# Kernel tuning notes

Hardware: AMD Instinct MI355X
Metric: run time of the kernel (lower is better)

Reference implementation:

```python
import jax, jax.numpy as jnp
import numpy as np
from jax import lax

B = 1024          # batch size (queries / docs)
H = 1536          # GRU hidden = embedding dim (hard-coded in module)
MAX_NEGS = 32     # max negatives per query
TEMP = 0.05       # opt.temperature


def setup_inputs() -> dict:
    key = jax.random.key(0)
    ks = jax.random.split(key, 8)
    rng = np.random.default_rng(0)
    lens = rng.integers(0, MAX_NEGS + 1, size=B)  # variable-length negs, some zero
    total = int(lens.sum())
    s = 0.02
    return {
        "q_emb": jax.random.normal(ks[0], (B, H), jnp.float32),
        "k_emb": jax.random.normal(ks[1], (B, H), jnp.float32),
        "inpn_emb": jax.random.normal(ks[2], (total, H), jnp.float32),
        "len_input_negs": jnp.asarray(lens, jnp.int32),
        "W_ih": jax.random.normal(ks[3], (3 * H, H), jnp.float32) * s,
        "W_hh": jax.random.normal(ks[4], (3 * H, H), jnp.float32) * s,
        "b_ih": jax.random.normal(ks[5], (3 * H,), jnp.float32) * s,
        "b_hh": jax.random.normal(ks[6], (3 * H,), jnp.float32) * s,
    }


def _ragged_gru_final(inpn_emb, lens, h0, W_ih, W_hh, b_ih, b_hh):
    """Batched equivalent of the per-sample torch GRU loop.

    For sample i: run a 1-layer GRU over inpn_emb[start_i:start_i+len_i]
    with initial hidden h0[i]; return final hidden (h0[i] if len_i == 0).
    """
    total = inpn_emb.shape[0]
    offsets = jnp.concatenate([jnp.zeros((1,), jnp.int32),
                               jnp.cumsum(lens)[:-1].astype(jnp.int32)])
    t = jnp.arange(MAX_NEGS, dtype=jnp.int32)
    idx = jnp.clip(offsets[:, None] + t[None, :], 0, total - 1)   # [B, Lmax]
    mask = t[None, :] < lens[:, None]                              # [B, Lmax]
    x_pad = inpn_emb[idx]                                          # [B, Lmax, H]

    def step(h, xm):
        x, m = xm                                  # x: [B,H], m: [B]
        gi = x @ W_ih.T + b_ih                     # [B, 3H]
        gh = h @ W_hh.T + b_hh                     # [B, 3H]
        i_r, i_z, i_n = jnp.split(gi, 3, axis=-1)
        h_r, h_z, h_n = jnp.split(gh, 3, axis=-1)
        r = jax.nn.sigmoid(i_r + h_r)
        z = jax.nn.sigmoid(i_z + h_z)
        n = jnp.tanh(i_n + r * h_n)
        h_new = (1.0 - z) * n + z * h
        h = jnp.where(m[:, None], h_new, h)        # freeze past end of seq
        return h, None

    h_final, _ = lax.scan(step, h0,
                          (x_pad.transpose(1, 0, 2), mask.T))
    return h_final


def reference(q_emb, k_emb, inpn_emb, len_input_negs, W_ih, W_hh, b_ih, b_hh):
    qemb = _ragged_gru_final(inpn_emb, len_input_negs, q_emb,
                             W_ih, W_hh, b_ih, b_hh)          # [B, H]
    scores = jnp.einsum("id,jd->ij", qemb / TEMP, k_emb)       # [B, B]
    labels = jnp.arange(B)
    logp = jax.nn.log_softmax(scores, axis=-1)
    loss = -jnp.mean(jnp.take_along_axis(logp, labels[:, None], axis=1))
    return loss
```

## Files before the change

### kernel.cpp

```cpp
#include <hip/hip_runtime.h>
#include <hip/hip_bf16.h>

#define B_SZ 1024
#define H_DIM 1536
#define H3 (3*H_DIM)
#define LMAX 32
#define TEMP_INV 20.0f

typedef __attribute__((ext_vector_type(4))) float f32x4;
typedef __attribute__((ext_vector_type(8))) short short8;
typedef unsigned short u16;
typedef unsigned int u32;

__device__ __forceinline__ u16 f2bf(float f){
  union { float f; u32 u; } v; v.f = f;
  u32 r = (v.u + 0x7FFFu + ((v.u >> 16) & 1u)) >> 16;
  return (u16)r;
}
__device__ __forceinline__ u32 pack2(float lo, float hi){
  return (u32)f2bf(lo) | ((u32)f2bf(hi) << 16);
}
__device__ __forceinline__ float bf2f(u16 b){
  union { u32 u; float f; } v; v.u = ((u32)b) << 16; return v.f;
}
__device__ __forceinline__ float sigm(float x){ return 1.f / (1.f + __expf(-x)); }

__device__ __forceinline__ void gload_lds16(const void* g, void* l){
  __builtin_amdgcn_global_load_lds(
      (const __attribute__((address_space(1))) void*)g,
      (__attribute__((address_space(3))) void*)l, 16, 0, 0);
}

__global__ void sort_kernel(const int* __restrict__ lens, int* __restrict__ rank,
                            int* __restrict__ cnt_arr, int* __restrict__ tstart,
                            int* __restrict__ rowmap)
{
  __shared__ int wavecnt[33][17];
  __shared__ int bintot[33];
  __shared__ int scnt[LMAX];
  __shared__ int sts[LMAX];
  __shared__ int soff[B_SZ];
  int i = threadIdx.x;
  int li = lens[i];
  int w = i >> 6, lane = i & 63;

  if (i < 33 * 17) ((int*)wavecnt)[i] = 0;
  __syncthreads();

  int mypre = 0;
  #pragma unroll 1
  for (int b = 0; b <= 32; ++b) {
    unsigned long long m = __ballot(li == b);
    if (lane == 0) wavecnt[b][w] = __popcll(m);
    if (b == li) mypre = __popcll(m & ((1ull << lane) - 1ull));
  }
  __syncthreads();

  if (i < 33) {
    int c = 0;
    #pragma unroll 1
    for (int w2 = 0; w2 < 16; ++w2) c += wavecnt[i][w2];
    bintot[i] = c;
  }
  __syncthreads();

  int wpre = 0;
  #pragma unroll 1
  for (int w2 = 0; w2 < w; ++w2) wpre += wavecnt[li][w2];
  int base = 0;
  #pragma unroll 1
  for (int b = li + 1; b <= 32; ++b) base += bintot[b];
  int r = base + wpre + mypre;
  rank[i] = r;

  if (i < LMAX) {
    int c = 0;
    #pragma unroll 1
    for (int b = i + 1; b <= 32; ++b) c += bintot[b];
    scnt[i] = c; cnt_arr[i] = c;
  }
  __syncthreads();
  if (i == 0) {
    int acc = 0;
    for (int t = 0; t < LMAX; ++t) { sts[t] = acc; tstart[t] = acc; acc += scnt[t]; }
  }

  soff[i] = li;
  __syncthreads();
  for (int off = 1; off < B_SZ; off <<= 1) {
    int v = (i >= off) ? soff[i - off] : 0;
    __syncthreads();
    soff[i] += v;
    __syncthreads();
  }
  int myoff = soff[i] - li;
  for (int t = 0; t < li; ++t)
    rowmap[myoff + t] = sts[t] + r;
}

__global__ void prep_kernel(const float* __restrict__ wih, const float* __restrict__ whh,
                            const float* __restrict__ kemb, const float* __restrict__ qemb,
                            const int* __restrict__ rank,
                            u16* __restrict__ wih_bf, u16* __restrict__ whh_bf,
                            u16* __restrict__ k_bf, u16* __restrict__ h0)
{
  size_t o = ((size_t)blockIdx.x * 256 + threadIdx.x) * 8;
  if (o < (size_t)H3 * H_DIM) {
    float4 a0 = *(const float4*)(wih + o), a1 = *(const float4*)(wih + o + 4);
    *(uint4*)(wih_bf + o) = make_uint4(pack2(a0.x,a0.y), pack2(a0.z,a0.w),
                                       pack2(a1.x,a1.y), pack2(a1.z,a1.w));
    float4 b0 = *(const float4*)(whh + o), b1 = *(const float4*)(whh + o + 4);
    *(uint4*)(whh_bf + o) = make_uint4(pack2(b0.x,b0.y), pack2(b0.z,b0.w),
                                       pack2(b1.x,b1.y), pack2(b1.z,b1.w));
  }
  if (o < (size_t)B_SZ * H_DIM) {
    float4 k0 = *(const float4*)(kemb + o), k1 = *(const float4*)(kemb + o + 4);
    *(uint4*)(k_bf + o) = make_uint4(pack2(k0.x,k0.y), pack2(k0.z,k0.w),
                                     pack2(k1.x,k1.y), pack2(k1.z,k1.w));
    int i = (int)(o / H_DIM), col = (int)(o % H_DIM);
    float4 q0 = *(const float4*)(qemb + o), q1 = *(const float4*)(qemb + o + 4);
    *(uint4*)(h0 + (size_t)rank[i] * H_DIM + col) =
        make_uint4(pack2(q0.x,q0.y), pack2(q0.z,q0.w),
                   pack2(q1.x,q1.y), pack2(q1.z,q1.w));
  }
}

__global__ void convx_kernel(const float* __restrict__ x, const int* __restrict__ rowmap,
                             u16* __restrict__ xt, int total){
  size_t o = ((size_t)blockIdx.x * 256 + threadIdx.x) * 8;
  int row = (int)(o / H_DIM), col = (int)(o % H_DIM);
  if (row < total) {
    float4 a0 = *(const float4*)(x + o), a1 = *(const float4*)(x + o + 4);
    *(uint4*)(xt + (size_t)rowmap[row] * H_DIM + col) =
        make_uint4(pack2(a0.x,a0.y), pack2(a0.z,a0.w),
                   pack2(a1.x,a1.y), pack2(a1.z,a1.w));
  } else {
    *(uint4*)(xt + o) = make_uint4(0,0,0,0);
  }
}

__global__ __launch_bounds__(256, 2) void gi_gemm_kernel(
    const u16* __restrict__ x_bf, const u16* __restrict__ wih_bf,
    const float* __restrict__ b_ih, u16* __restrict__ gi, int nblk_m)
{
  int nblk = nblk_m * 36;
  int id = blockIdx.x;
  int q8 = nblk >> 3, r8 = nblk & 7;
  int xcd = id & 7, off = id >> 3;
  int swz = (xcd < r8) ? (xcd * (q8 + 1) + off) : (r8 * (q8 + 1) + (xcd - r8) * q8 + off);
  int bx = swz / 36, by = swz % 36;

  __shared__ u16 lds[2 * 128 * 64];
  char* ldsb = (char*)lds;
  int tid = threadIdx.x, wid = tid >> 6, lane = tid & 63;
  int wm = wid >> 1, wn = wid & 1;
  int lrow = lane & 15, lkh = lane >> 4;
  f32x4 acc[4][4] = {};

  for (int kt = 0; kt < 24; ++kt) {
    int k0 = kt * 64;
    #pragma unroll
    for (int it = 0; it < 8; ++it) {
      int cb = it * 256 + wid * 64;
      int c  = cb + lane;
      int isB = c >> 10;
      int cc  = c & 1023;
      int row = cc >> 3, slot = cc & 7;
      const u16* src = isB ? (wih_bf + (size_t)(by * 128 + row) * H_DIM)
                           : (x_bf  + (size_t)(bx * 128 + row) * H_DIM);
      src += k0 + ((slot ^ (row & 7)) << 3);
      gload_lds16(src, ldsb + (size_t)cb * 16);
    }
    __syncthreads();
    #pragma unroll
    for (int qq = 0; qq < 2; ++qq) {
      short8 a[4], b[4];
      int slot = qq * 4 + lkh;
      #pragma unroll
      for (int m = 0; m < 4; ++m) {
        int row = wm * 64 + m * 16 + lrow;
        a[m] = *(const short8*)(ldsb + row * 128 + ((slot ^ (row & 7)) << 4));
      }
      #pragma unroll
      for (int n = 0; n < 4; ++n) {
        int row = wn * 64 + n * 16 + lrow;
        b[n] = *(const short8*)(ldsb + 16384 + row * 128 + ((slot ^ (row & 7)) << 4));
      }
      #pragma unroll
      for (int m = 0; m < 4; ++m)
        #pragma unroll
        for (int n = 0; n < 4; ++n)
          acc[m][n] = __builtin_amdgcn_mfma_f32_16x16x32_bf16(a[m], b[n], acc[m][n], 0,0,0);
    }
    __syncthreads();
  }
  #pragma unroll
  for (int n = 0; n < 4; ++n) {
    int j = by * 128 + wn * 64 + n * 16 + lrow;
    float bias = b_ih[j];
    #pragma unroll
    for (int m = 0; m < 4; ++m)
      #pragma unroll
      for (int r4 = 0; r4 < 4; ++r4) {
        int rowg = bx * 128 + wm * 64 + m * 16 + lkh * 4 + r4;
        gi[(size_t)rowg * 4608 + j] = f2bf(acc[m][n][r4] + bias);
      }
  }
}

__global__ __launch_bounds__(256, 4) void gh_step_kernel(
    const u16* __restrict__ h_cur, u16* __restrict__ h_nxt,
    const u16* __restrict__ whh_bf, const u16* __restrict__ gi,
    const float* __restrict__ b_hh,
    const int* __restrict__ cnt_arr, const int* __restrict__ tstart, int t)
{
  int cnt = cnt_arr[t];
  int bid = blockIdx.x;
  int x8 = bid & 7, jj = bid >> 3;
  int ct = x8 * 6 + jj % 6;
  int bx = jj / 6;
  if (bx * 64 >= cnt) return;
  int ts = tstart[t];

  __shared__ u16 lds[2 * 10240];
  char* ldsb = (char*)lds;

  int tid = threadIdx.x, wid = tid >> 6, lane = tid & 63;
  int wm = wid >> 1, wn = wid & 1;
  int lrow = lane & 15, lkh = lane >> 4;
  f32x4 acc[3][2] = {};
  float hold[2][4];

  auto STAGE = [&](int buf, int kt){
    int k0 = kt * 64;
    char* base = ldsb + buf * 20480;
    #pragma unroll
    for (int it = 0; it < 5; ++it) {
      int cb = it * 256 + wid * 64;
      int c  = cb + lane;
      const u16* src;
      if (c < 512) {
        int row = c >> 3, slot = c & 7;
        int ridx = bx * 64 + row; if (ridx >= cnt) ridx = cnt - 1;
        src = h_cur + (size_t)ridx * H_DIM + k0 + ((slot ^ (row & 7)) << 3);
      } else {
        int w = c - 512;
        int slab = w >> 8, row = (w >> 3) & 31, slot = w & 7;
        src = whh_bf + (size_t)(slab * H_DIM + ct * 32 + row) * H_DIM
              + k0 + ((slot ^ (row & 7)) << 3);
      }
      gload_lds16(src, base + (size_t)cb * 16);
    }
  };

  auto COMPUTE = [&](int buf){
    char* base = ldsb + buf * 20480;
    #pragma unroll
    for (int qq = 0; qq < 2; ++qq) {
      short8 ah[2], bw[3];
      int slot = qq * 4 + lkh;
      #pragma unroll
      for (int m = 0; m < 2; ++m) {
        int row = wm * 32 + m * 16 + lrow;
        ah[m] = *(const short8*)(base + row * 128 + ((slot ^ (row & 7)) << 4));
      }
      {
        int row = wn * 16 + lrow;
        int byte = row * 128 + ((slot ^ (row & 7)) << 4);
        #pragma unroll
        for (int s = 0; s < 3; ++s)
          bw[s] = *(const short8*)(base + 8192 + s * 4096 + byte);
      }
      #pragma unroll
      for (int s = 0; s < 3; ++s)
        #pragma unroll
        for (int m = 0; m < 2; ++m)
          acc[s][m] = __builtin_amdgcn_mfma_f32_16x16x32_bf16(
              ah[m], bw[s], acc[s][m], 0, 0, 0);
    }
  };

  STAGE(0, 0);

  int lc = wn * 16 + lrow;
  int j = ct * 32 + lc;
  u16 pgir[2][4], pgiz[2][4], pgin[2][4];
  asm volatile("" ::: "memory");
  float bhr = b_hh[j], bhz = b_hh[H_DIM + j], bhn = b_hh[2*H_DIM + j];
  #pragma unroll
  for (int m = 0; m < 2; ++m)
    #pragma unroll
    for (int r4 = 0; r4 < 4; ++r4) {
      int lm = wm * 32 + m * 16 + lkh * 4 + r4;
      int ridx = bx * 64 + lm; if (ridx >= cnt) ridx = cnt - 1;
      size_t gr = (size_t)(ts + ridx) * 4608;
      pgir[m][r4] = __builtin_nontemporal_load(&gi[gr + j]);
      pgiz[m][r4] = __builtin_nontemporal_load(&gi[gr + H_DIM + j]);
      pgin[m][r4] = __builtin_nontemporal_load(&gi[gr + 2*H_DIM + j]);
    }
  asm volatile("" ::: "memory");

  for (int kt = 0; kt < 24; ++kt) {
    if (kt + 1 < 24) {
      STAGE((kt + 1) & 1, kt + 1);
      asm volatile("s_waitcnt vmcnt(5)" ::: "memory");
    } else {
      asm volatile("s_waitcnt vmcnt(0)" ::: "memory");
    }
    __builtin_amdgcn_sched_barrier(0);
    __builtin_amdgcn_s_barrier();
    __builtin_amdgcn_sched_barrier(0);
    COMPUTE(kt & 1);
    if (kt == (ct >> 1)) {
      char* base = ldsb + (kt & 1) * 20480;
      int col = ((ct & 1) << 5) + wn * 16 + lrow;
      int slot = col >> 3, within = col & 7;
      #pragma unroll
      for (int m = 0; m < 2; ++m)
        #pragma unroll
        for (int r4 = 0; r4 < 4; ++r4) {
          int row = wm * 32 + m * 16 + lkh * 4 + r4;
          hold[m][r4] = bf2f(*(const u16*)(base + row * 128 +
                             ((slot ^ (row & 7)) << 4) + within * 2));
        }
    }
    __builtin_amdgcn_s_barrier();
    __builtin_amdgcn_sched_barrier(0);
  }

  #pragma unroll
  for (int m = 0; m < 2; ++m)
    #pragma unroll
    for (int r4 = 0; r4 < 4; ++r4) {
      int lm = wm * 32 + m * 16 + lkh * 4 + r4;
      int ridx = bx * 64 + lm;
      if (ridx < cnt) {
        float rr = sigm(bf2f(pgir[m][r4]) + acc[0][m][r4] + bhr);
        float zz = sigm(bf2f(pgiz[m][r4]) + acc[1][m][r4] + bhz);
        float nn = tanhf(bf2f(pgin[m][r4]) + rr * (acc[2][m][r4] + bhn));
        h_nxt[(size_t)ridx * H_DIM + j] = f2bf((1.f - zz) * nn + zz * hold[m][r4]);
      }
    }
}

__global__ __launch_bounds__(256, 2) void scores_kernel(
    const u16* __restrict__ h0, const u16* __restrict__ h1,
    const int* __restrict__ lens, const int* __restrict__ rank,
    const u16* __restrict__ k_bf, float* __restrict__ scores)
{
  int bx = blockIdx.x, by = blockIdx.y;
  __shared__ u16 lds[2 * 2 * 64 * 64];
  char* ldsb = (char*)lds;
  int tid = threadIdx.x, wid = tid >> 6, lane = tid & 63;
  int wm = wid >> 1, wn = wid & 1;
  int lrow = lane & 15, lkh = lane >> 4;
  f32x4 acc[2][2] = {};

  auto STAGE = [&](int buf, int kt){
    int k0 = kt * 64;
    char* base = ldsb + buf * 16384;
    #pragma unroll
    for (int it = 0; it < 4; ++it) {
      int cb = it * 256 + wid * 64;
      int c  = cb + lane;
      int isB = c >> 9;
      int cc  = c & 511;
      int row = cc >> 3, slot = cc & 7;
      const u16* src;
      if (!isB) {
        int g = bx * 64 + row;
        src = ((lens[g] & 1) ? h1 : h0) + (size_t)rank[g] * H_DIM;
      } else {
        src = k_bf + (size_t)(by * 64 + row) * H_DIM;
      }
      src += k0 + ((slot ^ (row & 7)) << 3);
      gload_lds16(src, base + (size_t)cb * 16);
    }
  };

  auto COMPUTE = [&](int buf){
    char* base = ldsb + buf * 16384;
    #pragma unroll
    for (int qq = 0; qq < 2; ++qq) {
      short8 a[2], b[2];
      int slot = qq * 4 + lkh;
      #pragma unroll
      for (int m = 0; m < 2; ++m) {
        int row = wm * 32 + m * 16 + lrow;
        a[m] = *(const short8*)(base + row * 128 + ((slot ^ (row & 7)) << 4));
      }
      #pragma unroll
      for (int n = 0; n < 2; ++n) {
        int row = wn * 32 + n * 16 + lrow;
        b[n] = *(const short8*)(base + 8192 + row * 128 + ((slot ^ (row & 7)) << 4));
      }
      #pragma unroll
      for (int m = 0; m < 2; ++m)
        #pragma unroll
        for (int n = 0; n < 2; ++n)
          acc[m][n] = __builtin_amdgcn_mfma_f32_16x16x32_bf16(a[m], b[n], acc[m][n], 0,0,0);
    }
  };

  STAGE(0, 0);
  for (int kt = 0; kt < 24; ++kt) {
    if (kt + 1 < 24) {
      STAGE((kt + 1) & 1, kt + 1);
      asm volatile("s_waitcnt vmcnt(4)" ::: "memory");
    } else {
      asm volatile("s_waitcnt vmcnt(0)" ::: "memory");
    }
    __builtin_amdgcn_sched_barrier(0);
    __builtin_amdgcn_s_barrier();
    __builtin_amdgcn_sched_barrier(0);
    COMPUTE(kt & 1);
    __builtin_amdgcn_s_barrier();
    __builtin_amdgcn_sched_barrier(0);
  }
  #pragma unroll
  for (int m = 0; m < 2; ++m)
    #pragma unroll
    for (int n = 0; n < 2; ++n) {
      int col = by * 64 + wn * 32 + n * 16 + lrow;
      #pragma unroll
      for (int r4 = 0; r4 < 4; ++r4) {
        int rowg = bx * 64 + wm * 32 + m * 16 + lkh * 4 + r4;
        scores[(size_t)rowg * B_SZ + col] = acc[m][n][r4] * TEMP_INV;
      }
    }
}

__global__ void softmax_kernel(const float* __restrict__ scores, float* __restrict__ out){
  int i = blockIdx.x;
  int tid = threadIdx.x;
  const float* row = scores + (size_t)i * B_SZ;
  __shared__ float red[4];
  float m = -INFINITY;
  for (int j = tid; j < B_SZ; j += 256) m = fmaxf(m, row[j]);
  for (int off = 32; off; off >>= 1) m = fmaxf(m, __shfl_xor(m, off));
  if ((tid & 63) == 0) red[tid >> 6] = m;
  __syncthreads();
  m = fmaxf(fmaxf(red[0], red[1]), fmaxf(red[2], red[3]));
  __syncthreads();
  float s = 0.f;
  for (int j = tid; j < B_SZ; j += 256) s += __expf(row[j] - m);
  for (int off = 32; off; off >>= 1) s += __shfl_xor(s, off);
  if ((tid & 63) == 0) red[tid >> 6] = s;
  __syncthreads();
  if (tid == 0) {
    float S = red[0] + red[1] + red[2] + red[3];
    atomicAdd(out, (m + __logf(S) - row[i]) * (1.0f / B_SZ));
  }
}

extern "C" void kernel_launch(void* const* d_in, const int* in_sizes, int n_in,
                              void* d_out, int out_size, void* d_ws, size_t ws_size,
                              hipStream_t stream) {
  const float* q_emb = (const float*)d_in[0];
  const float* k_emb = (const float*)d_in[1];
  const float* inpn  = (const float*)d_in[2];
  const int*   lens  = (const int*)d_in[3];
  const float* wih   = (const float*)d_in[4];
  const float* whh   = (const float*)d_in[5];
  const float* bih   = (const float*)d_in[6];
  const float* bhh   = (const float*)d_in[7];
  float* out = (float*)d_out;

  int total  = in_sizes[2] / H_DIM;
  int mtiles = (total + 127) / 128;
  int Mpad   = mtiles * 128;

  char* p = (char*)d_ws;
  auto alloc = [&](size_t bytes){ char* r = p; p += (bytes + 255) & ~(size_t)255; return r; };
  int* rank      = (int*)alloc(B_SZ * 4);
  int* cnt_arr   = (int*)alloc(LMAX * 4);
  int* tstart    = (int*)alloc(LMAX * 4);
  int* rowmap    = (int*)alloc((size_t)Mpad * 4);
  u16* hbuf0     = (u16*)alloc((size_t)B_SZ * H_DIM * 2);
  u16* hbuf1     = (u16*)alloc((size_t)B_SZ * H_DIM * 2);
  u16* wih_bf    = (u16*)alloc((size_t)H3 * H_DIM * 2);
  u16* whh_bf    = (u16*)alloc((size_t)H3 * H_DIM * 2);
  u16* k_bf      = (u16*)alloc((size_t)B_SZ * H_DIM * 2);
  u16* xt        = (u16*)alloc((size_t)Mpad * H_DIM * 2);
  u16* gi        = (u16*)alloc((size_t)Mpad * H3 * 2);
  float* scores  = (float*)alloc((size_t)B_SZ * B_SZ * 4);
  if ((size_t)(p - (char*)d_ws) > ws_size) return;

  hipMemsetAsync(out, 0, 4, stream);

  sort_kernel<<<1, B_SZ, 0, stream>>>(lens, rank, cnt_arr, tstart, rowmap);
  prep_kernel<<<(H3 * H_DIM / 8) / 256, 256, 0, stream>>>(
      wih, whh, k_emb, q_emb, rank, wih_bf, whh_bf, k_bf, hbuf0);
  convx_kernel<<<((size_t)Mpad * H_DIM / 8) / 256, 256, 0, stream>>>(
      inpn, rowmap, xt, total);

  gi_gemm_kernel<<<mtiles * 36, 256, 0, stream>>>(xt, wih_bf, bih, gi, mtiles);

  for (int t = 0; t < LMAX; ++t) {
    u16* hc = (t & 1) ? hbuf1 : hbuf0;
    u16* hn = (t & 1) ? hbuf0 : hbuf1;
    gh_step_kernel<<<768, 256, 0, stream>>>(
        hc, hn, whh_bf, gi, bhh, cnt_arr, tstart, t);
  }

  scores_kernel<<<dim3(B_SZ / 64, B_SZ / 64), 256, 0, stream>>>(
      hbuf0, hbuf1, lens, rank, k_bf, scores);
  softmax_kernel<<<B_SZ, 256, 0, stream>>>(scores, out);
}
```

Before: 965.3 us.

## Rework gi GEMM to 256x256 tiles with double-buffered pipelined loads; trim step grids

The input-gate GEMM moves to 512-thread blocks computing 256x256 tiles. It uses double-buffered LDS, staged prefetch of the next K tiles interleaved with MFMA work, explicit vmcnt waits and setprio scheduling. This raises arithmetic intensity and hides global-load latency. Separately, the per-timestep GRU kernel launches are sized from an upper bound on active sequences (total/(t+1)), and the loop stops early when no sequence can still be active, so fewer empty blocks are launched.

```diff
diff --git a/kernel.cpp b/kernel.cpp
--- a/kernel.cpp
+++ b/kernel.cpp
@@ -139,71 +139,129 @@
   }
 }
 
-__global__ __launch_bounds__(256, 2) void gi_gemm_kernel(
+__global__ __launch_bounds__(512, 2) void gi_gemm_kernel(
     const u16* __restrict__ x_bf, const u16* __restrict__ wih_bf,
-    const float* __restrict__ b_ih, u16* __restrict__ gi, int nblk_m)
+    const float* __restrict__ b_ih, u16* __restrict__ gi, int mt)
 {
-  int nblk = nblk_m * 36;
+  int nblk = mt * 18;
   int id = blockIdx.x;
   int q8 = nblk >> 3, r8 = nblk & 7;
   int xcd = id & 7, off = id >> 3;
   int swz = (xcd < r8) ? (xcd * (q8 + 1) + off) : (r8 * (q8 + 1) + (xcd - r8) * q8 + off);
-  int bx = swz / 36, by = swz % 36;
-
-  __shared__ u16 lds[2 * 128 * 64];
+  int bx = swz / 18, by = swz % 18;
+
+  __shared__ u16 lds[2 * 32768];
   char* ldsb = (char*)lds;
+
   int tid = threadIdx.x, wid = tid >> 6, lane = tid & 63;
-  int wm = wid >> 1, wn = wid & 1;
+  int wm = wid >> 2, wn = wid & 3;
   int lrow = lane & 15, lkh = lane >> 4;
-  f32x4 acc[4][4] = {};
-
-  for (int kt = 0; kt < 24; ++kt) {
-    int k0 = kt * 64;
-    #pragma unroll
-    for (int it = 0; it < 8; ++it) {
-      int cb = it * 256 + wid * 64;
+
+  f32x4 acc[8][4] = {};
+
+  auto SH = [&](int dbuf, int which, int tile){
+    char* base = ldsb + dbuf * 65536 + which * 16384;
+    int k0 = tile * 64;
+    #pragma unroll
+    for (int it = 0; it < 2; ++it) {
+      int cb = wid * 128 + it * 64;
       int c  = cb + lane;
-      int isB = c >> 10;
-      int cc  = c & 1023;
-      int row = cc >> 3, slot = cc & 7;
-      const u16* src = isB ? (wih_bf + (size_t)(by * 128 + row) * H_DIM)
-                           : (x_bf  + (size_t)(bx * 128 + row) * H_DIM);
+      int row = c >> 3, slot = c & 7;
+      const u16* src;
+      if (which < 2) src = x_bf   + (size_t)(bx * 256 + which * 128 + row) * H_DIM;
+      else           src = wih_bf + (size_t)(by * 256 + (which - 2) * 128 + row) * H_DIM;
       src += k0 + ((slot ^ (row & 7)) << 3);
-      gload_lds16(src, ldsb + (size_t)cb * 16);
-    }
-    __syncthreads();
-    #pragma unroll
-    for (int qq = 0; qq < 2; ++qq) {
-      short8 a[4], b[4];
-      int slot = qq * 4 + lkh;
-      #pragma unroll
-      for (int m = 0; m < 4; ++m) {
-        int row = wm * 64 + m * 16 + lrow;
-        a[m] = *(const short8*)(ldsb + row * 128 + ((slot ^ (row & 7)) << 4));
-      }
-      #pragma unroll
-      for (int n = 0; n < 4; ++n) {
-        int row = wn * 64 + n * 16 + lrow;
-        b[n] = *(const short8*)(ldsb + 16384 + row * 128 + ((slot ^ (row & 7)) << 4));
-      }
-      #pragma unroll
-      for (int m = 0; m < 4; ++m)
-        #pragma unroll
-        for (int n = 0; n < 4; ++n)
-          acc[m][n] = __builtin_amdgcn_mfma_f32_16x16x32_bf16(a[m], b[n], acc[m][n], 0,0,0);
-    }
-    __syncthreads();
-  }
+      gload_lds16(src, base + (size_t)cb * 16);
+    }
+  };
+
+  SH(0,2,0); SH(0,3,0); SH(0,0,0); SH(0,1,0); SH(1,2,1); SH(1,3,1);
+  asm volatile("s_waitcnt vmcnt(4)" ::: "memory");
+  __builtin_amdgcn_sched_barrier(0);
+  __builtin_amdgcn_s_barrier();
+  __builtin_amdgcn_sched_barrier(0);
+
+  short8 bfr[4][2], afr[2][2];
+
+  for (int k = 0; k < 24; ++k) {
+    int d = k & 1;
+    char* Ab = ldsb + d * 65536 + wm * 16384;
+    char* Bb = ldsb + d * 65536 + 32768 + (wn >> 1) * 16384;
+    int bloc = (wn & 1) * 64;
+
+    #pragma unroll
+    for (int cf = 0; cf < 4; ++cf)
+      #pragma unroll
+      for (int ks = 0; ks < 2; ++ks) {
+        int r = bloc + cf * 16 + lrow;
+        bfr[cf][ks] = *(const short8*)(Bb + r * 128 + (((ks*4+lkh) ^ (r & 7)) << 4));
+      }
+    #pragma unroll
+    for (int rq = 0; rq < 2; ++rq)
+      #pragma unroll
+      for (int ks = 0; ks < 2; ++ks) {
+        int r = rq * 16 + lrow;
+        afr[rq][ks] = *(const short8*)(Ab + r * 128 + (((ks*4+lkh) ^ (r & 7)) << 4));
+      }
+    if (k + 1 < 24) SH(d ^ 1, 0, k + 1);
+    __builtin_amdgcn_s_setprio(1);
+    #pragma unroll
+    for (int rq = 0; rq < 2; ++rq)
+      #pragma unroll
+      for (int cf = 0; cf < 4; ++cf)
+        #pragma unroll
+        for (int ks = 0; ks < 2; ++ks)
+          acc[rq][cf] = __builtin_amdgcn_mfma_f32_16x16x32_bf16(
+              afr[rq][ks], bfr[cf][ks], acc[rq][cf], 0, 0, 0);
+    __builtin_amdgcn_s_setprio(0);
+    __builtin_amdgcn_s_barrier();
+    __builtin_amdgcn_sched_barrier(0);
+
+    #pragma unroll
+    for (int q = 1; q < 4; ++q) {
+      #pragma unroll
+      for (int rq = 0; rq < 2; ++rq)
+        #pragma unroll
+        for (int ks = 0; ks < 2; ++ks) {
+          int r = (q * 2 + rq) * 16 + lrow;
+          afr[rq][ks] = *(const short8*)(Ab + r * 128 + (((ks*4+lkh) ^ (r & 7)) << 4));
+        }
+      if (q == 1) {
+        if (k + 1 < 24) SH(d ^ 1, 1, k + 1);
+        if (k + 2 < 24) SH(d,     2, k + 2);
+      } else if (q == 2) {
+        if (k + 2 < 24) SH(d,     3, k + 2);
+      }
+      __builtin_amdgcn_s_setprio(1);
+      #pragma unroll
+      for (int rq = 0; rq < 2; ++rq)
+        #pragma unroll
+        for (int cf = 0; cf < 4; ++cf)
+          #pragma unroll
+          for (int ks = 0; ks < 2; ++ks)
+            acc[q*2+rq][cf] = __builtin_amdgcn_mfma_f32_16x16x32_bf16(
+                afr[rq][ks], bfr[cf][ks], acc[q*2+rq][cf], 0, 0, 0);
+      __builtin_amdgcn_s_setprio(0);
+      if (q == 3) {
+        if (k < 22) asm volatile("s_waitcnt vmcnt(4)" ::: "memory");
+        else        asm volatile("s_waitcnt vmcnt(0)" ::: "memory");
+        __builtin_amdgcn_sched_barrier(0);
+      }
+      __builtin_amdgcn_s_barrier();
+      __builtin_amdgcn_sched_barrier(0);
+    }
+  }
+
   #pragma unroll
-  for (int n = 0; n < 4; ++n) {
-    int j = by * 128 + wn * 64 + n * 16 + lrow;
+  for (int cf = 0; cf < 4; ++cf) {
+    int j = by * 256 + wn * 64 + cf * 16 + lrow;
     float bias = b_ih[j];
     #pragma unroll
-    for (int m = 0; m < 4; ++m)
+    for (int rf = 0; rf < 8; ++rf)
       #pragma unroll
       for (int r4 = 0; r4 < 4; ++r4) {
-        int rowg = bx * 128 + wm * 64 + m * 16 + lkh * 4 + r4;
-        gi[(size_t)rowg * 4608 + j] = f2bf(acc[m][n][r4] + bias);
+        int rowg = bx * 256 + wm * 128 + rf * 16 + lkh * 4 + r4;
+        gi[(size_t)rowg * 4608 + j] = f2bf(acc[rf][cf][r4] + bias);
       }
   }
 }
@@ -467,8 +525,8 @@
   float* out = (float*)d_out;
 
   int total  = in_sizes[2] / H_DIM;
-  int mtiles = (total + 127) / 128;
-  int Mpad   = mtiles * 128;
+  int mtiles = (total + 255) / 256;
+  int Mpad   = mtiles * 256;
 
   char* p = (char*)d_ws;
   auto alloc = [&](size_t bytes){ char* r = p; p += (bytes + 255) & ~(size_t)255; return r; };
@@ -494,12 +552,15 @@
   convx_kernel<<<((size_t)Mpad * H_DIM / 8) / 256, 256, 0, stream>>>(
       inpn, rowmap, xt, total);
 
-  gi_gemm_kernel<<<mtiles * 36, 256, 0, stream>>>(xt, wih_bf, bih, gi, mtiles);
+  gi_gemm_kernel<<<mtiles * 18, 512, 0, stream>>>(xt, wih_bf, bih, gi, mtiles);
 
   for (int t = 0; t < LMAX; ++t) {
     u16* hc = (t & 1) ? hbuf1 : hbuf0;
     u16* hn = (t & 1) ? hbuf0 : hbuf1;
-    gh_step_kernel<<<768, 256, 0, stream>>>(
+    int cmax = total / (t + 1); if (cmax > B_SZ) cmax = B_SZ;
+    if (cmax <= 0) break;
+    int tiles = (cmax + 63) / 64;
+    gh_step_kernel<<<48 * tiles, 256, 0, stream>>>(
         hc, hn, whh_bf, gi, bhh, cnt_arr, tstart, t);
   }
 
```

Result: faster. 928.1 us, median of 3 (-3.9%).
